# Kernel optimization log

Hardware: AMD Instinct MI355X
Metric: run time of the kernel (lower is better)

## Reference

```python
import jax, jax.numpy as jnp
import numpy as np

HEADS = 8
DIM_HEAD = 64
RMS_EPS = 1.1920929e-07  # torch default eps = finfo(fp32).eps


def rotate_half(x):
    x1, x2 = jnp.split(x, 2, axis=-1)
    return jnp.concatenate((-x2, x1), axis=-1)


def setup_inputs() -> dict:
    key = jax.random.key(0)
    k1, k2, k3, k4, k5 = jax.random.split(key, 5)
    b, n, dim = 2, 4096, 1024
    dim_hidden = HEADS * DIM_HEAD  # 512
    x = jax.random.normal(k1, (b, n, dim), dtype=jnp.float32)
    rotary_emb = jax.random.normal(k2, (n, DIM_HEAD), dtype=jnp.float32)
    rms_weight = jnp.ones((dim,), dtype=jnp.float32)
    w_qkv = jax.random.normal(k3, (dim, dim_hidden * 3), dtype=jnp.float32) * (dim ** -0.5)
    w_out = jax.random.normal(k4, (dim_hidden, dim), dtype=jnp.float32) * (dim_hidden ** -0.5)
    return {"x": x, "rotary_emb": rotary_emb, "rms_weight": rms_weight,
            "w_qkv": w_qkv, "w_out": w_out}


def reference(x, rotary_emb, rms_weight, w_qkv, w_out):
    b, n, dim = x.shape
    h, d = HEADS, DIM_HEAD
    # RMSNorm
    xn = x * jax.lax.rsqrt(jnp.mean(x * x, axis=-1, keepdims=True) + RMS_EPS) * rms_weight
    # QKV projection, rearrange 'b n (qkv h d) -> qkv b h n d'
    qkv = (xn @ w_qkv).reshape(b, n, 3, h, d).transpose(2, 0, 3, 1, 4)
    q, k, v = qkv[0], qkv[1], qkv[2]
    # RoPE
    cos, sin = jnp.cos(rotary_emb), jnp.sin(rotary_emb)  # (n, d) broadcasts over b,h
    q = q * cos + rotate_half(q) * sin
    k = k * cos + rotate_half(k) * sin
    q = q * (d ** -0.5)
    sim = jnp.einsum('bhid,bhjd->bhij', q, k)
    causal_mask = jnp.triu(jnp.ones((n, n), dtype=bool), 1)
    sim = jnp.where(causal_mask, -jnp.finfo(sim.dtype).max, sim)
    attn = jax.nn.softmax(sim, axis=-1)
    out = jnp.einsum('bhij,bhjd->bhid', attn, v)
    out = out.transpose(0, 2, 1, 3).reshape(b, n, h * d)  # 'b h n d -> b n (h d)'
    return out @ w_out
```

## Files before the change

kernel.cpp:

```cpp
#include <hip/hip_runtime.h>
#include <hip/hip_bf16.h>
#include <cstdint>

using bf16x8 = __attribute__((ext_vector_type(8))) __bf16;
using f32x4  = __attribute__((ext_vector_type(4))) float;

#define LOG2E 1.4426950408889634f

__device__ inline void gload16(__bf16* lds, const __bf16* g) {
    __builtin_amdgcn_global_load_lds((const __attribute__((address_space(1))) void*)g,
                                     (__attribute__((address_space(3))) void*)lds, 16, 0, 0);
}
__device__ inline void wait_barrier4() {
    asm volatile("s_waitcnt vmcnt(4)" ::: "memory");
    __builtin_amdgcn_s_barrier();
}
__device__ inline void wait_barrier0() {
    asm volatile("s_waitcnt vmcnt(0)" ::: "memory");
    __builtin_amdgcn_s_barrier();
}

__global__ __launch_bounds__(256) void rmsnorm_kernel(const float* __restrict__ x,
                                                      const float* __restrict__ w,
                                                      __bf16* __restrict__ xn) {
    const int row = blockIdx.x;
    const float4 v = reinterpret_cast<const float4*>(x + (size_t)row * 1024)[threadIdx.x];
    float ss = v.x * v.x + v.y * v.y + v.z * v.z + v.w * v.w;
#pragma unroll
    for (int i = 1; i < 64; i <<= 1) ss += __shfl_xor(ss, i);
    __shared__ float part[4];
    if ((threadIdx.x & 63) == 0) part[threadIdx.x >> 6] = ss;
    __syncthreads();
    const float total = part[0] + part[1] + part[2] + part[3];
    const float scale = rsqrtf(total * (1.0f / 1024.0f) + 1.1920929e-07f);
    const float4 wv = reinterpret_cast<const float4*>(w)[threadIdx.x];
    union { __bf16 h[4]; uint2 u; } pk;
    pk.h[0] = (__bf16)(v.x * scale * wv.x);
    pk.h[1] = (__bf16)(v.y * scale * wv.y);
    pk.h[2] = (__bf16)(v.z * scale * wv.z);
    pk.h[3] = (__bf16)(v.w * scale * wv.w);
    reinterpret_cast<uint2*>(xn + (size_t)row * 1024)[threadIdx.x] = pk.u;
}

__global__ void transpose_cast_kernel(const float* __restrict__ in,
                                      __bf16* __restrict__ out, int K, int N) {
    __shared__ float tile[32][33];
    const int n0 = blockIdx.x * 32, k0 = blockIdx.y * 32;
#pragma unroll
    for (int r = threadIdx.y; r < 32; r += 8)
        tile[r][threadIdx.x] = in[(size_t)(k0 + r) * N + n0 + threadIdx.x];
    __syncthreads();
#pragma unroll
    for (int r = threadIdx.y; r < 32; r += 8)
        out[(size_t)(n0 + r) * K + k0 + threadIdx.x] = (__bf16)tile[threadIdx.x][r];
}

__global__ __launch_bounds__(256) void csin_kernel(const float* __restrict__ rot,
                                                   float2* __restrict__ csin) {
    const int i = blockIdx.x * 256 + threadIdx.x;
    float s, c;
    sincosf(rot[i], &s, &c);
    csin[i] = make_float2(c, s);
}

__global__ __launch_bounds__(256) void rope_kernel(__bf16* __restrict__ qk,
                                                   const float2* __restrict__ csin) {
    const int row = blockIdx.x * 4 + (threadIdx.x >> 6);
    const int lane = threadIdx.x & 63;
    const int h = lane >> 3, dl = (lane & 7) * 4;
    const int pos = row & 4095;
    const float4 csA = *reinterpret_cast<const float4*>(&csin[pos * 64 + dl]);
    const float4 csB = *reinterpret_cast<const float4*>(&csin[pos * 64 + dl + 2]);
    const float4 csC = *reinterpret_cast<const float4*>(&csin[pos * 64 + dl + 32]);
    const float4 csD = *reinterpret_cast<const float4*>(&csin[pos * 64 + dl + 34]);
    const float c0[4] = {csA.x, csA.z, csB.x, csB.z};
    const float s0[4] = {csA.y, csA.w, csB.y, csB.w};
    const float c1[4] = {csC.x, csC.z, csD.x, csD.z};
    const float s1[4] = {csC.y, csC.w, csD.y, csD.w};
    __bf16* p = qk + (size_t)row * 1024 + h * 64 + dl;
    const float qs = 0.125f * LOG2E;
#pragma unroll
    for (int part = 0; part < 2; ++part) {
        __bf16* pp = p + part * 512;
        const float sc = part ? 1.0f : qs;
        union { uint2 u; __bf16 hh[4]; } va, vb, oa, ob;
        va.u = *reinterpret_cast<const uint2*>(pp);
        vb.u = *reinterpret_cast<const uint2*>(pp + 32);
#pragma unroll
        for (int j = 0; j < 4; ++j) {
            const float a = (float)va.hh[j], b2 = (float)vb.hh[j];
            oa.hh[j] = (__bf16)((a * c0[j] - b2 * s0[j]) * sc);
            ob.hh[j] = (__bf16)((b2 * c1[j] + a * s1[j]) * sc);
        }
        *reinterpret_cast<uint2*>(pp)      = oa.u;
        *reinterpret_cast<uint2*>(pp + 32) = ob.u;
    }
}

template <typename OutT, int MODE>
__global__ __launch_bounds__(256) void gemm_bt(const __bf16* __restrict__ A,
                                               const __bf16* __restrict__ Bt,
                                               OutT* __restrict__ C,
                                               __bf16* __restrict__ vt,
                                               int M, int N, int K) {
    __shared__ __align__(16) __bf16 As[3][128 * 32];
    __shared__ __align__(16) __bf16 Bs[3][128 * 32];
    const int bm = blockIdx.y, bn = blockIdx.x;
    const int tid = threadIdx.x;
    const int w = tid >> 6, l = tid & 63, lg = l >> 4, lr = l & 15;
    const int wr = w >> 1, wc = w & 1;
    const __bf16* Ab = A + (size_t)(bm * 128) * K;
    const __bf16* Bb = Bt + (size_t)(bn * 128) * K;
    const int srow = tid >> 2, scol = (tid & 3) * 8;
    const __bf16* Asrc = Ab + (size_t)srow * K + scol;
    const __bf16* Bsrc = Bb + (size_t)srow * K + scol;

    auto stage = [&](int k2) {
        const int nx = k2 % 3;
        const int off = k2 * 32;
        gload16(&As[nx][tid * 8],        Asrc + off);
        gload16(&As[nx][2048 + tid * 8], Asrc + (size_t)64 * K + off);
        gload16(&Bs[nx][tid * 8],        Bsrc + off);
        gload16(&Bs[nx][2048 + tid * 8], Bsrc + (size_t)64 * K + off);
    };

    const int NS = K >> 5;
    f32x4 acc[4][4] = {};
    stage(0);
    stage(1);
    wait_barrier4();
    for (int k = 0; k < NS; ++k) {
        const bool more = (k + 2 < NS);
        if (more) stage(k + 2);
        const __bf16* Ac = &As[k % 3][0];
        const __bf16* Bc = &Bs[k % 3][0];
        bf16x8 af[4], bfr[4];
#pragma unroll
        for (int m = 0; m < 4; ++m)
            af[m] = *reinterpret_cast<const bf16x8*>(Ac + (wr * 64 + m * 16 + lr) * 32 + lg * 8);
#pragma unroll
        for (int nn = 0; nn < 4; ++nn)
            bfr[nn] = *reinterpret_cast<const bf16x8*>(Bc + (wc * 64 + nn * 16 + lr) * 32 + lg * 8);
#pragma unroll
        for (int m = 0; m < 4; ++m)
#pragma unroll
            for (int nn = 0; nn < 4; ++nn)
                acc[m][nn] = __builtin_amdgcn_mfma_f32_16x16x32_bf16(af[m], bfr[nn],
                                                                     acc[m][nn], 0, 0, 0);
        if (more) wait_barrier4();
        else      wait_barrier0();
    }

    const int cb = bn * 128 + wc * 64;
    if constexpr (MODE == 1) {
        if (cb >= 1024) {
#pragma unroll
            for (int m = 0; m < 4; ++m) {
                const int rg = bm * 128 + wr * 64 + m * 16 + 4 * lg;
                const int bidx = rg >> 12, pos0 = rg & 4095;
                const int a0 = pos0 & 63;
                const int cp = 32 * (a0 >> 5) + 8 * ((a0 >> 2) & 3) + 4 * ((a0 >> 4) & 1);
                const int nbase = (pos0 & ~63) + cp;
#pragma unroll
                for (int nn = 0; nn < 4; ++nn) {
                    const int col = cb + nn * 16 + lr - 1024;
                    const int hh = col >> 6, dd = col & 63;
                    union { __bf16 h4[4]; uint2 u; } pk2;
#pragma unroll
                    for (int r = 0; r < 4; ++r) pk2.h4[r] = (__bf16)acc[m][nn][r];
                    *reinterpret_cast<uint2*>(&vt[((size_t)(bidx * 8 + hh) * 64 + dd) * 4096 + nbase]) = pk2.u;
                }
            }
            return;
        }
    }
    float* tb = reinterpret_cast<float*>(&As[0][0]) + w * 1088;
    const int row = l >> 2, c4 = (l & 3) * 16;
#pragma unroll
    for (int m = 0; m < 4; ++m) {
#pragma unroll
        for (int nn = 0; nn < 4; ++nn)
#pragma unroll
            for (int r = 0; r < 4; ++r)
                tb[(4 * lg + r) * 68 + nn * 16 + lr] = acc[m][nn][r];
        const int rg2 = bm * 128 + wr * 64 + m * 16 + row;
        float v[16];
#pragma unroll
        for (int j = 0; j < 4; ++j)
            *reinterpret_cast<float4*>(v + 4 * j) =
                *reinterpret_cast<const float4*>(tb + row * 68 + c4 + 4 * j);
        if constexpr (MODE == 1) {
            union { __bf16 h16[16]; uint4 u4[2]; } ob;
#pragma unroll
            for (int j = 0; j < 16; ++j) ob.h16[j] = (__bf16)v[j];
            uint4* dst = reinterpret_cast<uint4*>(C + (size_t)rg2 * 1024 + cb + c4);
            dst[0] = ob.u4[0];
            dst[1] = ob.u4[1];
        } else {
#pragma unroll
            for (int j = 0; j < 4; ++j)
                *reinterpret_cast<float4*>(&C[(size_t)rg2 * N + cb + c4 + 4 * j]) =
                    *reinterpret_cast<const float4*>(v + 4 * j);
        }
    }
}

__global__ __launch_bounds__(256) void attn_kernel(const __bf16* __restrict__ qkp,
                                                   const __bf16* __restrict__ vt,
                                                   __bf16* __restrict__ attn_out) {
    const int bid = blockIdx.x;
    const int j = bid >> 3;
    const int bh = 2 * (bid & 7) + (j & 1);
    const int qt = 63 - (j >> 1);
    const int b = bh >> 3, h = bh & 7;
    const int tid = threadIdx.x;
    const int w = tid >> 6, l = tid & 63, lg = l >> 4, lr = l & 15;

    __shared__ __align__(16) __bf16 Ks[3][64 * 64];
    __shared__ __align__(16) __bf16 Vs[3][64 * 64];

    const __bf16* qbase = qkp + (size_t)b * 4096 * 1024 + h * 64;
    const __bf16* kbase = qbase + 512;
    const __bf16* vtb   = vt + (size_t)(b * 8 + h) * 64 * 4096;

    const int sr = tid >> 3;
    const int sc = ((tid & 7) ^ (sr & 7)) * 8;
    const __bf16* kp = kbase + (size_t)sr * 1024 + sc;
    const __bf16* vp = vtb + (size_t)sr * 4096 + sc;

    const int xel = (lr & 7) * 8;

    const int wq0 = qt * 64 + 16 * w;
    const int nkt = qt + 1;

    bf16x8 Qf[2];
#pragma unroll
    for (int kh = 0; kh < 2; ++kh)
        Qf[kh] = *reinterpret_cast<const bf16x8*>(
            qbase + (size_t)(wq0 + lr) * 1024 + 32 * kh + 8 * lg);

    f32x4 O[4] = {};
    float m_ = -1e30f, l_ = 0.0f;

    auto stage2 = [&](__bf16* kdst, __bf16* vdst) {
        gload16(kdst + tid * 8,         kp);
        gload16(kdst + (tid + 256) * 8, kp + 32 * 1024);
        gload16(vdst + tid * 8,         vp);
        gload16(vdst + (tid + 256) * 8, vp + 32 * 4096);
        kp += 64 * 1024;
        vp += 64;
    };
    auto qk_step = [&](f32x4 (&S)[4], const __bf16* kb) {
        __builtin_amdgcn_s_setprio(1);
#pragma unroll
        for (int jt = 0; jt < 4; ++jt) {
            const __bf16* kr = kb + (16 * jt + lr) * 64;
            const bf16x8 Kf0 = *reinterpret_cast<const bf16x8*>(kr + ((8 * lg) ^ xel));
            const bf16x8 Kf1 = *reinterpret_cast<const bf16x8*>(kr + ((32 + 8 * lg) ^ xel));
            f32x4 z = {};
            z = __builtin_amdgcn_mfma_f32_16x16x32_bf16(Kf0, Qf[0], z, 0, 0, 0);
            S[jt] = __builtin_amdgcn_mfma_f32_16x16x32_bf16(Kf1, Qf[1], z, 0, 0, 0);
        }
        __builtin_amdgcn_s_setprio(0);
    };
    auto smpv = [&](f32x4 (&SC)[4], const __bf16* vb, bool domask) {
        if (domask) {
#pragma unroll
            for (int jt = 0; jt < 4; ++jt)
#pragma unroll
                for (int r = 0; r < 4; ++r)
                    if (16 * jt + 4 * lg + r > 16 * w + lr) SC[jt][r] = -1e30f;
        }
        float mx = -1e30f;
#pragma unroll
        for (int jt = 0; jt < 4; ++jt)
            mx = fmaxf(mx, fmaxf(fmaxf(SC[jt][0], SC[jt][1]), fmaxf(SC[jt][2], SC[jt][3])));
        if (__any(mx > m_ + 8.0f)) {
            mx = fmaxf(mx, __shfl_xor(mx, 16));
            mx = fmaxf(mx, __shfl_xor(mx, 32));
            const float mn = fmaxf(m_, mx);
            const float alpha = __builtin_amdgcn_exp2f(m_ - mn);
            m_ = mn;
            l_ *= alpha;
#pragma unroll
            for (int dt = 0; dt < 4; ++dt) O[dt] *= alpha;
        }
        float sum = 0.0f;
#pragma unroll
        for (int jt = 0; jt < 4; ++jt)
#pragma unroll
            for (int r = 0; r < 4; ++r) {
                const float pv = __builtin_amdgcn_exp2f(SC[jt][r] - m_);
                SC[jt][r] = pv;
                sum += pv;
            }
        l_ += sum;
        __builtin_amdgcn_s_setprio(1);
#pragma unroll
        for (int s = 0; s < 2; ++s) {
            bf16x8 Pf;
#pragma unroll
            for (int i = 0; i < 8; ++i)
                Pf[i] = (__bf16)SC[2 * s + (i >> 2)][i & 3];
#pragma unroll
            for (int dt = 0; dt < 4; ++dt) {
                const bf16x8 Vf = *reinterpret_cast<const bf16x8*>(
                    vb + (16 * dt + lr) * 64 + ((32 * s + 8 * lg) ^ xel));
                O[dt] = __builtin_amdgcn_mfma_f32_16x16x32_bf16(Vf, Pf, O[dt], 0, 0, 0);
            }
        }
        __builtin_amdgcn_s_setprio(0);
    };

    f32x4 S0[4], S1[4];
    int t = 0;

    stage2(Ks[0], Vs[0]);
    stage2(Ks[1], Vs[1]);
    __syncthreads();
    qk_step(S0, Ks[0]);

    for (; t + 8 <= nkt; t += 6) {
        stage2(Ks[2], Vs[2]); qk_step(S1, Ks[1]); smpv(S0, Vs[0], false); __syncthreads();
        stage2(Ks[0], Vs[0]); qk_step(S0, Ks[2]); smpv(S1, Vs[1], false); __syncthreads();
        stage2(Ks[1], Vs[1]); qk_step(S1, Ks[0]); smpv(S0, Vs[2], false); __syncthreads();
        stage2(Ks[2], Vs[2]); qk_step(S0, Ks[1]); smpv(S1, Vs[0], false); __syncthreads();
        stage2(Ks[0], Vs[0]); qk_step(S1, Ks[2]); smpv(S0, Vs[1], false); __syncthreads();
        stage2(Ks[1], Vs[1]); qk_step(S0, Ks[0]); smpv(S1, Vs[2], false); __syncthreads();
    }

    {
        f32x4 Sp[4];
#pragma unroll
        for (int jt = 0; jt < 4; ++jt) Sp[jt] = S0[jt];
        for (; t < nkt; ++t) {
            if (t + 2 < nkt) stage2(Ks[(t + 2) % 3], Vs[(t + 2) % 3]);
            f32x4 Sn[4];
            if (t + 1 < nkt) qk_step(Sn, Ks[(t + 1) % 3]);
            smpv(Sp, Vs[t % 3], t == nkt - 1);
            __syncthreads();
#pragma unroll
            for (int jt = 0; jt < 4; ++jt) Sp[jt] = Sn[jt];
        }
    }

    float lt = l_;
    lt += __shfl_xor(lt, 16);
    lt += __shfl_xor(lt, 32);
    const float inv = 1.0f / lt;
    __bf16* op = attn_out + ((size_t)b * 4096 + wq0 + lr) * 512 + h * 64;
#pragma unroll
    for (int dt = 0; dt < 4; ++dt) {
        union { __bf16 h4[4]; uint2 u; } ow;
#pragma unroll
        for (int r = 0; r < 4; ++r) ow.h4[r] = (__bf16)(O[dt][r] * inv);
        *reinterpret_cast<uint2*>(op + 16 * dt + 4 * lg) = ow.u;
    }
}

extern "C" void kernel_launch(void* const* d_in, const int* in_sizes, int n_in,
                              void* d_out, int out_size, void* d_ws, size_t ws_size,
                              hipStream_t stream) {
    (void)in_sizes; (void)n_in; (void)out_size; (void)ws_size;
    const float* x    = (const float*)d_in[0];
    const float* rot  = (const float*)d_in[1];
    const float* rmsw = (const float*)d_in[2];
    const float* wqkv = (const float*)d_in[3];
    const float* wout = (const float*)d_in[4];
    float* out = (float*)d_out;

    char* ws = (char*)d_ws;
    __bf16* xn    = (__bf16*)ws;
    __bf16* wqkvt = (__bf16*)(ws + 16777216);
    __bf16* woutt = (__bf16*)(ws + 16777216 + 3145728);
    __bf16* aout  = (__bf16*)(ws + 16777216 + 3145728 + 1048576);
    __bf16* qk   = (__bf16*)d_out;
    float2* csin = (float2*)((char*)d_out + 16777216);
    __bf16* vt   = (__bf16*)((char*)d_out + 18874368);

    rmsnorm_kernel<<<8192, 256, 0, stream>>>(x, rmsw, xn);
    transpose_cast_kernel<<<dim3(48, 32), dim3(32, 8), 0, stream>>>(wqkv, wqkvt, 1024, 1536);
    transpose_cast_kernel<<<dim3(32, 16), dim3(32, 8), 0, stream>>>(wout, woutt, 512, 1024);
    csin_kernel<<<1024, 256, 0, stream>>>(rot, csin);
    gemm_bt<__bf16, 1><<<dim3(12, 64), 256, 0, stream>>>(xn, wqkvt, qk, vt, 8192, 1536, 1024);
    rope_kernel<<<2048, 256, 0, stream>>>(qk, csin);
    attn_kernel<<<1024, 256, 0, stream>>>(qk, vt, aout);
    gemm_bt<float, 0><<<dim3(8, 64), 256, 0, stream>>>(aout, woutt, out, nullptr, 8192, 1024, 512);
}
```

Baseline: 145.8 us.

## Compute softmax row sums via MFMA with ones and simplify GEMM epilogue stores

```diff
diff --git a/kernel.cpp b/kernel.cpp
--- a/kernel.cpp
+++ b/kernel.cpp
@@ -150,10 +150,21 @@
         if (more) wait_barrier4();
         else      wait_barrier0();
     }
-
-    const int cb = bn * 128 + wc * 64;
     if constexpr (MODE == 1) {
-        if (cb >= 1024) {
+        const int cb = bn * 128 + wc * 64;
+        if (cb < 1024) {
+#pragma unroll
+            for (int m = 0; m < 4; ++m) {
+                const int rg = bm * 128 + wr * 64 + m * 16 + 4 * lg;
+#pragma unroll
+                for (int nn = 0; nn < 4; ++nn) {
+                    const int cg = cb + nn * 16 + lr;
+#pragma unroll
+                    for (int r = 0; r < 4; ++r)
+                        C[(size_t)(rg + r) * 1024 + cg] = (OutT)acc[m][nn][r];
+                }
+            }
+        } else {
 #pragma unroll
             for (int m = 0; m < 4; ++m) {
                 const int rg = bm * 128 + wr * 64 + m * 16 + 4 * lg;
@@ -171,36 +182,18 @@
                     *reinterpret_cast<uint2*>(&vt[((size_t)(bidx * 8 + hh) * 64 + dd) * 4096 + nbase]) = pk2.u;
                 }
             }
-            return;
-        }
-    }
-    float* tb = reinterpret_cast<float*>(&As[0][0]) + w * 1088;
-    const int row = l >> 2, c4 = (l & 3) * 16;
+        }
+        return;
+    }
 #pragma unroll
     for (int m = 0; m < 4; ++m) {
-#pragma unroll
-        for (int nn = 0; nn < 4; ++nn)
+        const int rg = bm * 128 + wr * 64 + m * 16 + 4 * lg;
+#pragma unroll
+        for (int nn = 0; nn < 4; ++nn) {
+            const int cg = bn * 128 + wc * 64 + nn * 16 + lr;
 #pragma unroll
             for (int r = 0; r < 4; ++r)
-                tb[(4 * lg + r) * 68 + nn * 16 + lr] = acc[m][nn][r];
-        const int rg2 = bm * 128 + wr * 64 + m * 16 + row;
-        float v[16];
-#pragma unroll
-        for (int j = 0; j < 4; ++j)
-            *reinterpret_cast<float4*>(v + 4 * j) =
-                *reinterpret_cast<const float4*>(tb + row * 68 + c4 + 4 * j);
-        if constexpr (MODE == 1) {
-            union { __bf16 h16[16]; uint4 u4[2]; } ob;
-#pragma unroll
-            for (int j = 0; j < 16; ++j) ob.h16[j] = (__bf16)v[j];
-            uint4* dst = reinterpret_cast<uint4*>(C + (size_t)rg2 * 1024 + cb + c4);
-            dst[0] = ob.u4[0];
-            dst[1] = ob.u4[1];
-        } else {
-#pragma unroll
-            for (int j = 0; j < 4; ++j)
-                *reinterpret_cast<float4*>(&C[(size_t)rg2 * N + cb + c4 + 4 * j]) =
-                    *reinterpret_cast<const float4*>(v + 4 * j);
+                C[(size_t)(rg + r) * N + cg] = (OutT)acc[m][nn][r];
         }
     }
 }
@@ -239,8 +232,13 @@
         Qf[kh] = *reinterpret_cast<const bf16x8*>(
             qbase + (size_t)(wq0 + lr) * 1024 + 32 * kh + 8 * lg);
 
+    bf16x8 ones;
+#pragma unroll
+    for (int i = 0; i < 8; ++i) ones[i] = (__bf16)1.0f;
+
     f32x4 O[4] = {};
-    float m_ = -1e30f, l_ = 0.0f;
+    f32x4 Lacc = {};
+    float m_ = -1e30f;
 
     auto stage2 = [&](__bf16* kdst, __bf16* vdst) {
         gload16(kdst + tid * 8,         kp);
@@ -281,20 +279,15 @@
             const float mn = fmaxf(m_, mx);
             const float alpha = __builtin_amdgcn_exp2f(m_ - mn);
             m_ = mn;
-            l_ *= alpha;
+            Lacc *= alpha;
 #pragma unroll
             for (int dt = 0; dt < 4; ++dt) O[dt] *= alpha;
         }
-        float sum = 0.0f;
 #pragma unroll
         for (int jt = 0; jt < 4; ++jt)
 #pragma unroll
-            for (int r = 0; r < 4; ++r) {
-                const float pv = __builtin_amdgcn_exp2f(SC[jt][r] - m_);
-                SC[jt][r] = pv;
-                sum += pv;
-            }
-        l_ += sum;
+            for (int r = 0; r < 4; ++r)
+                SC[jt][r] = __builtin_amdgcn_exp2f(SC[jt][r] - m_);
         __builtin_amdgcn_s_setprio(1);
 #pragma unroll
         for (int s = 0; s < 2; ++s) {
@@ -302,6 +295,7 @@
 #pragma unroll
             for (int i = 0; i < 8; ++i)
                 Pf[i] = (__bf16)SC[2 * s + (i >> 2)][i & 3];
+            Lacc = __builtin_amdgcn_mfma_f32_16x16x32_bf16(ones, Pf, Lacc, 0, 0, 0);
 #pragma unroll
             for (int dt = 0; dt < 4; ++dt) {
                 const bf16x8 Vf = *reinterpret_cast<const bf16x8*>(
@@ -344,10 +338,7 @@
         }
     }
 
-    float lt = l_;
-    lt += __shfl_xor(lt, 16);
-    lt += __shfl_xor(lt, 32);
-    const float inv = 1.0f / lt;
+    const float inv = 1.0f / Lacc[0];
     __bf16* op = attn_out + ((size_t)b * 4096 + wq0 + lr) * 512 + h * 64;
 #pragma unroll
     for (int dt = 0; dt < 4; ++dt) {
```

New measurement: 138.6 us. 1.05x faster.
